# Kernel optimization log

Hardware: AMD Instinct MI355X
Metric: run time of the kernel (lower is better)

Reference implementation:

```python
import jax, jax.numpy as jnp
import numpy as np

NUM_HEADS = 8


def _forward(x, Wq, bq, Wk, bk, Wv, bv, Wo, bo, w1, b1, w2, b2, tau):
    B, S, E = x.shape
    H = NUM_HEADS
    hd = E // H
    scale = hd ** -0.5

    def heads(t):
        return t.reshape(B, S, H, hd).transpose(0, 2, 1, 3)  # [B,H,S,hd]

    q = heads(x @ Wq + bq)
    k = heads(x @ Wk + bk)
    v = heads(x @ Wv + bv)
    s = jnp.einsum('bhqd,bhkd->bhqk', q, k) * scale  # [B,H,S,S]

    # ---- autopoietic transform (vectorized over batch, no mask) ----
    s = jnp.clip(jnp.nan_to_num(s, nan=0.0, posinf=10.0, neginf=-10.0), -15.0, 15.0)
    ma = s.mean(axis=1)  # mean over heads -> [B,S,S]
    eps_safe = 0.05  # clamp(eps=1e-6, 0.05, 0.8)
    sa = jnp.clip(jnp.clip(ma, -8.0, 8.0) * eps_safe, -10.0, 10.0)
    # 1x1 conv on [1,1,S,S] == per-channel scalar scale+bias -> [B,C,S,S]
    hid = jax.nn.relu(jnp.clip(sa[:, None] * w1[None, :, None, None]
                               + b1[None, :, None, None], -5.0, 5.0))
    ap = jnp.clip(jnp.einsum('bcij,c->bij', hid, w2) + b2, -5.0, 5.0)
    taylor = jnp.clip(1.0 + 0.05 * (ap * 50.0), 0.5, 1.5)
    sig = jax.nn.sigmoid(taylor)
    p = jax.nn.softmax(jnp.clip(ma, -10.0, 10.0), axis=-1)
    Hent = -p * jnp.log(p + 1e-6)
    Fm = jax.nn.softmax(3.0 * Hent, axis=-1)
    t = sig * Fm
    eo = jnp.sqrt((ma * ma).sum(axis=(1, 2), keepdims=True)) + 1e-4  # fro norm
    et = jnp.sqrt((t * t).sum(axis=(1, 2), keepdims=True)) + 1e-4
    t = jnp.clip(eo / et, 0.8, 1.2) * t
    tm = t.mean(axis=(1, 2), keepdims=True)
    om = ma.mean(axis=(1, 2), keepdims=True)
    tstd = jnp.sqrt(jnp.clip(((t - tm) ** 2).mean(axis=(1, 2), keepdims=True), 0.01, None))
    ostd = jnp.sqrt(jnp.clip(((ma - om) ** 2).mean(axis=(1, 2), keepdims=True), 0.01, None))
    gd = jnp.clip(ostd / tstd, 0.8, 1.2)
    ar = jnp.clip(jnp.abs(ma).max(axis=(1, 2), keepdims=True), 1.0, 10.0)
    sm = jnp.clip(0.3 / jnp.log1p(ar), 0.1, 0.5)
    st = tm + sm * gd * (t - tm)  # scaled_transform
    ent = Hent.mean(axis=(1, 2), keepdims=True)
    ne = ent / jnp.log(jnp.float32(S))  # normalized entropy (max_entropy = log S)
    rr = 0.4 * (1.0 - jnp.clip(ne, 0.0, 0.4))  # residual ratio (base 0.4, entropy-damped)
    # blend transform back into per-head scores (res_scale = 1.0)
    s = s + rr[:, None] * (st - ma)[:, None]

    attn = jax.nn.softmax(s / tau, axis=-1)
    out = jnp.einsum('bhqk,bhkd->bhqd', attn, v)
    out = out.transpose(0, 2, 1, 3).reshape(B, S, E)
    return out @ Wo + bo


def setup_inputs() -> dict:
    key = jax.random.key(0)
    ks = jax.random.split(key, 8)
    B, S, E, C = 4, 512, 512, 128
    w_scale = 0.02
    return {
        'x': jax.random.normal(ks[0], (B, S, E), dtype=jnp.float32),
        'Wq': jax.random.normal(ks[1], (E, E), dtype=jnp.float32) * w_scale,
        'bq': jnp.zeros((E,), jnp.float32),
        'Wk': jax.random.normal(ks[2], (E, E), dtype=jnp.float32) * w_scale,
        'bk': jnp.zeros((E,), jnp.float32),
        'Wv': jax.random.normal(ks[3], (E, E), dtype=jnp.float32) * w_scale,
        'bv': jnp.zeros((E,), jnp.float32),
        'Wo': jax.random.normal(ks[4], (E, E), dtype=jnp.float32) * w_scale,
        'bo': jnp.zeros((E,), jnp.float32),
        'w1': jax.random.normal(ks[5], (C,), dtype=jnp.float32) * 0.5,
        'b1': jnp.zeros((C,), jnp.float32),
        'w2': jax.random.normal(ks[6], (C,), dtype=jnp.float32) * 0.1,
        'b2': jnp.zeros((1,), jnp.float32),
        'tau': jnp.ones((1,), jnp.float32),
    }


def reference(x, Wq, bq, Wk, bk, Wv, bv, Wo, bo, w1, b1, w2, b2, tau):
    return _forward(x, Wq, bq, Wk, bk, Wv, bv, Wo, bo, w1, b1, w2, b2, tau)
```

## Files before the change

kernel.cpp:

```cpp
#include <hip/hip_runtime.h>
#include <math.h>

#define BB 4
#define SS 512
#define EE 512
#define NH 8
#define HD 64
#define NC 128
#define NTAB 4096

typedef _Float16 f16x8 __attribute__((ext_vector_type(8)));
typedef float f32x4 __attribute__((ext_vector_type(4)));

struct HL { _Float16 h, l; };

__device__ __forceinline__ float clampf(float v, float lo, float hi) {
  return fminf(fmaxf(v, lo), hi);
}
__device__ __forceinline__ HL split16(float x) {
  HL r;
  r.h = (_Float16)x;
  r.l = (_Float16)(x - (float)r.h);
  return r;
}

__device__ __forceinline__ float waveRedSum(float v) {
#pragma unroll
  for (int o = 32; o; o >>= 1) v += __shfl_xor(v, o);
  return v;
}
__device__ __forceinline__ float waveRedMax(float v) {
#pragma unroll
  for (int o = 32; o; o >>= 1) v = fmaxf(v, __shfl_xor(v, o));
  return v;
}
__device__ __forceinline__ float blockRedSum(float v, float* red) {
  int tid = threadIdx.x;
  v = waveRedSum(v);
  __syncthreads();
  if ((tid & 63) == 0) red[tid >> 6] = v;
  __syncthreads();
  return red[0] + red[1] + red[2] + red[3];
}
__device__ __forceinline__ float blockRedMax(float v, float* red) {
  int tid = threadIdx.x;
  v = waveRedMax(v);
  __syncthreads();
  if ((tid & 63) == 0) red[tid >> 6] = v;
  __syncthreads();
  return fmaxf(fmaxf(red[0], red[1]), fmaxf(red[2], red[3]));
}

__global__ __launch_bounds__(256) void k_prep(
    const float* __restrict__ Wq, const float* __restrict__ Wk,
    const float* __restrict__ Wv, const float* __restrict__ Wo,
    _Float16* __restrict__ Wth, _Float16* __restrict__ Wtl) {
  const int j = blockIdx.x;
  const int tid = threadIdx.x;
  const int z = j >> 6;
  const int rem = j & 63;
  const int k0 = (rem & 7) * 64, n0 = (rem >> 3) * 64;
  const float* W = (z == 0) ? Wq : (z == 1) ? Wk : (z == 2) ? Wv : Wo;
  __shared__ float Tt[64][68];
  const int r = tid >> 2, c = (tid & 3) * 16;
#pragma unroll
  for (int jj = 0; jj < 16; jj += 4)
    *(float4*)&Tt[r][c + jj] =
        *(const float4*)(W + (size_t)(k0 + r) * EE + n0 + c + jj);
  __syncthreads();
  f16x8 h0, l0, h1, l1;
#pragma unroll
  for (int jj = 0; jj < 8; ++jj) {
    HL r0 = split16(Tt[c + jj][r]);
    HL r1 = split16(Tt[c + 8 + jj][r]);
    h0[jj] = r0.h; l0[jj] = r0.l;
    h1[jj] = r1.h; l1[jj] = r1.l;
  }
  _Float16* dh = Wth + ((size_t)z * EE + n0 + r) * EE + k0 + c;
  _Float16* dl = Wtl + ((size_t)z * EE + n0 + r) * EE + k0 + c;
  *(f16x8*)dh = h0;
  *(f16x8*)(dh + 8) = h1;
  *(f16x8*)dl = l0;
  *(f16x8*)(dl + 8) = l1;
}

__global__ __launch_bounds__(256) void k_qkv_mfma(
    const float* __restrict__ x,
    const _Float16* __restrict__ Wth, const _Float16* __restrict__ Wtl,
    const float* __restrict__ bq, const float* __restrict__ bk,
    const float* __restrict__ bv, const float* __restrict__ w1,
    const float* __restrict__ b1, const float* __restrict__ w2,
    const float* __restrict__ b2, float* __restrict__ T,
    _Float16* __restrict__ qh,
    _Float16* __restrict__ kh, _Float16* __restrict__ kl,
    _Float16* __restrict__ vth, _Float16* __restrict__ vtl) {
  const int which = blockIdx.z;
  const int tid = threadIdx.x;
  const int wave = tid >> 6, lane = tid & 63;
  const int quad = lane >> 4, l16 = lane & 15;
  const int m0 = blockIdx.y * 64;
  const int n0 = blockIdx.x * 64;
  const _Float16* Bh = Wth + (size_t)which * EE * EE;
  const _Float16* Bl = Wtl + (size_t)which * EE * EE;

  __shared__ __align__(16) char smpool[27648];
  _Float16(*LAh)[72] = (_Float16(*)[72])(smpool);
  _Float16(*LBh)[72] = (_Float16(*)[72])(smpool + 9216);
  _Float16(*LBl)[72] = (_Float16(*)[72])(smpool + 18432);
  float(*TR)[68] = (float(*)[68])(smpool);

  const int sr0 = tid >> 3, sc0 = (tid & 7) * 8;
  const int sr1 = sr0 + 32;

  float4 rx0a = *(const float4*)(x + (size_t)(m0 + sr0) * EE + sc0);
  float4 rx0b = *(const float4*)(x + (size_t)(m0 + sr0) * EE + sc0 + 4);
  float4 rx1a = *(const float4*)(x + (size_t)(m0 + sr1) * EE + sc0);
  float4 rx1b = *(const float4*)(x + (size_t)(m0 + sr1) * EE + sc0 + 4);
  f16x8 rB0h = *(const f16x8*)(Bh + (size_t)(n0 + sr0) * EE + sc0);
  f16x8 rB0l = *(const f16x8*)(Bl + (size_t)(n0 + sr0) * EE + sc0);
  f16x8 rB1h = *(const f16x8*)(Bh + (size_t)(n0 + sr1) * EE + sc0);
  f16x8 rB1l = *(const f16x8*)(Bl + (size_t)(n0 + sr1) * EE + sc0);

  f32x4 acc[4] = {};
  for (int k0 = 0; k0 < EE; k0 += 64) {
    if (k0) __syncthreads();
    {
      float f0[8] = {rx0a.x, rx0a.y, rx0a.z, rx0a.w,
                     rx0b.x, rx0b.y, rx0b.z, rx0b.w};
      float f1[8] = {rx1a.x, rx1a.y, rx1a.z, rx1a.w,
                     rx1b.x, rx1b.y, rx1b.z, rx1b.w};
      f16x8 h0, h1;
#pragma unroll
      for (int j = 0; j < 8; ++j) {
        h0[j] = (_Float16)f0[j];
        h1[j] = (_Float16)f1[j];
      }
      *(f16x8*)&LAh[sr0][sc0] = h0;
      *(f16x8*)&LAh[sr1][sc0] = h1;
    }
    *(f16x8*)&LBh[sr0][sc0] = rB0h;
    *(f16x8*)&LBl[sr0][sc0] = rB0l;
    *(f16x8*)&LBh[sr1][sc0] = rB1h;
    *(f16x8*)&LBl[sr1][sc0] = rB1l;
    __syncthreads();
    if (k0 + 64 < EE) {
      const int kn = k0 + 64;
      rx0a = *(const float4*)(x + (size_t)(m0 + sr0) * EE + kn + sc0);
      rx0b = *(const float4*)(x + (size_t)(m0 + sr0) * EE + kn + sc0 + 4);
      rx1a = *(const float4*)(x + (size_t)(m0 + sr1) * EE + kn + sc0);
      rx1b = *(const float4*)(x + (size_t)(m0 + sr1) * EE + kn + sc0 + 4);
      rB0h = *(const f16x8*)(Bh + (size_t)(n0 + sr0) * EE + kn + sc0);
      rB0l = *(const f16x8*)(Bl + (size_t)(n0 + sr0) * EE + kn + sc0);
      rB1h = *(const f16x8*)(Bh + (size_t)(n0 + sr1) * EE + kn + sc0);
      rB1l = *(const f16x8*)(Bl + (size_t)(n0 + sr1) * EE + kn + sc0);
    }
#pragma unroll
    for (int kk = 0; kk < 64; kk += 32) {
      f16x8 ah = *(const f16x8*)&LAh[wave * 16 + l16][kk + quad * 8];
#pragma unroll
      for (int nt = 0; nt < 4; ++nt) {
        f16x8 bhf = *(const f16x8*)&LBh[nt * 16 + l16][kk + quad * 8];
        f16x8 blf = *(const f16x8*)&LBl[nt * 16 + l16][kk + quad * 8];
        acc[nt] = __builtin_amdgcn_mfma_f32_16x16x32_f16(ah, bhf, acc[nt], 0, 0, 0);
        acc[nt] = __builtin_amdgcn_mfma_f32_16x16x32_f16(ah, blf, acc[nt], 0, 0, 0);
      }
    }
  }
  const float* bias = (which == 0) ? bq : (which == 1) ? bk : bv;
  if (which == 2) {
    __syncthreads();
#pragma unroll
    for (int nt = 0; nt < 4; ++nt) {
      const int dcol = nt * 16 + l16;
      const float bb = bias[n0 + nt * 16 + l16];
#pragma unroll
      for (int r = 0; r < 4; ++r)
        TR[dcol][wave * 16 + quad * 4 + r] = acc[nt][r] + bb;
    }
    __syncthreads();
    const int d = tid >> 2, cc = (tid & 3) * 16;
    const int bh = (m0 >> 9) * NH + (n0 >> 6);
    const int si0 = m0 & 511;
    f16x8 h0, l0, h1, l1;
#pragma unroll
    for (int jj = 0; jj < 8; ++jj) {
      HL r0 = split16(TR[d][cc + jj]);
      HL r1 = split16(TR[d][cc + 8 + jj]);
      h0[jj] = r0.h; l0[jj] = r0.l;
      h1[jj] = r1.h; l1[jj] = r1.l;
    }
    _Float16* dh = vth + ((size_t)bh * HD + d) * SS + si0 + cc;
    _Float16* dl = vtl + ((size_t)bh * HD + d) * SS + si0 + cc;
    *(f16x8*)dh = h0;
    *(f16x8*)(dh + 8) = h1;
    *(f16x8*)dl = l0;
    *(f16x8*)(dl + 8) = l1;
  } else {
    const float postscale = (which == 0) ? 0.125f : 1.0f;
    const int mbase = m0 + wave * 16 + quad * 4;
#pragma unroll
    for (int nt = 0; nt < 4; ++nt) {
      const int col = n0 + nt * 16 + l16;
      const float bb = bias[col];
#pragma unroll
      for (int r = 0; r < 4; ++r) {
        const size_t idx = (size_t)(mbase + r) * EE + col;
        const float val = (acc[nt][r] + bb) * postscale;
        if (which == 0) {
          qh[idx] = (_Float16)val;
        } else {
          HL sp = split16(val);
          kh[idx] = sp.h;
          kl[idx] = sp.l;
        }
      }
    }
    if (which == 0 && blockIdx.x == 0 && blockIdx.y < 17) {
      int idx = blockIdx.y * 256 + tid;
      if (idx <= NTAB) {
        float sa = -0.4f + (float)idx * (0.8f / (float)NTAB);
        float ap = 0.f;
#pragma unroll 4
        for (int c = 0; c < NC; ++c) {
          float h = fminf(fmaxf(sa * w1[c] + b1[c], 0.f), 5.f);
          ap += h * w2[c];
        }
        ap = clampf(ap + b2[0], -5.f, 5.f);
        float tay = clampf(1.0f + 0.05f * (ap * 50.0f), 0.5f, 1.5f);
        T[idx] = 1.0f / (1.0f + expf(-tay));
      }
    }
  }
}

__global__ __launch_bounds__(256) void k_ma_mfma(
    const _Float16* __restrict__ qh,
    const _Float16* __restrict__ kh, const _Float16* __restrict__ kl,
    float* __restrict__ ma) {
  const int tid = threadIdx.x;
  const int wave = tid >> 6, lane = tid & 63;
  const int quad = lane >> 4, l16 = lane & 15;
  const int m0 = blockIdx.y * 64;
  const int n0 = blockIdx.x * 64;
  const _Float16* Bh = kh + (size_t)(m0 >> 9) * SS * EE;
  const _Float16* Bl = kl + (size_t)(m0 >> 9) * SS * EE;

  __shared__ _Float16 LAh[64][72], LBh[64][72], LBl[64][72];

  const int sr0 = tid >> 3, sc0 = (tid & 7) * 8;
  const int sr1 = sr0 + 32;

  f16x8 rA0h = *(const f16x8*)(qh + (size_t)(m0 + sr0) * EE + sc0);
  f16x8 rB0h = *(const f16x8*)(Bh + (size_t)(n0 + sr0) * EE + sc0);
  f16x8 rB0l = *(const f16x8*)(Bl + (size_t)(n0 + sr0) * EE + sc0);
  f16x8 rA1h = *(const f16x8*)(qh + (size_t)(m0 + sr1) * EE + sc0);
  f16x8 rB1h = *(const f16x8*)(Bh + (size_t)(n0 + sr1) * EE + sc0);
  f16x8 rB1l = *(const f16x8*)(Bl + (size_t)(n0 + sr1) * EE + sc0);

  f32x4 acc[4] = {};
  for (int k0 = 0; k0 < EE; k0 += 64) {
    if (k0) __syncthreads();
    *(f16x8*)&LAh[sr0][sc0] = rA0h;
    *(f16x8*)&LBh[sr0][sc0] = rB0h;
    *(f16x8*)&LBl[sr0][sc0] = rB0l;
    *(f16x8*)&LAh[sr1][sc0] = rA1h;
    *(f16x8*)&LBh[sr1][sc0] = rB1h;
    *(f16x8*)&LBl[sr1][sc0] = rB1l;
    __syncthreads();
    if (k0 + 64 < EE) {
      const int kn = k0 + 64;
      rA0h = *(const f16x8*)(qh + (size_t)(m0 + sr0) * EE + kn + sc0);
      rB0h = *(const f16x8*)(Bh + (size_t)(n0 + sr0) * EE + kn + sc0);
      rB0l = *(const f16x8*)(Bl + (size_t)(n0 + sr0) * EE + kn + sc0);
      rA1h = *(const f16x8*)(qh + (size_t)(m0 + sr1) * EE + kn + sc0);
      rB1h = *(const f16x8*)(Bh + (size_t)(n0 + sr1) * EE + kn + sc0);
      rB1l = *(const f16x8*)(Bl + (size_t)(n0 + sr1) * EE + kn + sc0);
    }
#pragma unroll
    for (int kk = 0; kk < 64; kk += 32) {
      f16x8 ah = *(const f16x8*)&LAh[wave * 16 + l16][kk + quad * 8];
#pragma unroll
      for (int nt = 0; nt < 4; ++nt) {
        f16x8 bhf = *(const f16x8*)&LBh[nt * 16 + l16][kk + quad * 8];
        f16x8 blf = *(const f16x8*)&LBl[nt * 16 + l16][kk + quad * 8];
        acc[nt] = __builtin_amdgcn_mfma_f32_16x16x32_f16(ah, bhf, acc[nt], 0, 0, 0);
        acc[nt] = __builtin_amdgcn_mfma_f32_16x16x32_f16(ah, blf, acc[nt], 0, 0, 0);
      }
    }
  }
  const int mbase = m0 + wave * 16 + quad * 4;
#pragma unroll
  for (int nt = 0; nt < 4; ++nt) {
    const int col = n0 + nt * 16 + l16;
#pragma unroll
    for (int r = 0; r < 4; ++r) {
      ma[(size_t)(mbase + r) * SS + col] = acc[nt][r] * 0.125f;
    }
  }
}

__global__ __launch_bounds__(256) void k_rowstat(
    const float* __restrict__ ma, const float* __restrict__ T,
    float* __restrict__ t_un, float* __restrict__ rowred) {
  const int row = blockIdx.x * 4 + (threadIdx.x >> 6);
  const int lane = threadIdx.x & 63;

  const float4* p =
      reinterpret_cast<const float4*>(ma + (size_t)row * SS) + lane * 2;
  float4 u0 = p[0], u1 = p[1];
  float m[8] = {u0.x, u0.y, u0.z, u0.w, u1.x, u1.y, u1.z, u1.w};

  float sma = 0.f, sma2 = 0.f, mabs = 0.f;
#pragma unroll
  for (int e = 0; e < 8; ++e) {
    sma += m[e];
    sma2 += m[e] * m[e];
    mabs = fmaxf(mabs, fabsf(m[e]));
  }
  sma = waveRedSum(sma);
  sma2 = waveRedSum(sma2);
  mabs = waveRedMax(mabs);

  float ex[8], esum = 0.f;
#pragma unroll
  for (int e = 0; e < 8; ++e) {
    ex[e] = __expf(clampf(m[e], -10.f, 10.f));
    esum += ex[e];
  }
  esum = waveRedSum(esum);
  float inv = 1.0f / esum;
  float Hv[8], sH = 0.f;
#pragma unroll
  for (int e = 0; e < 8; ++e) {
    float pp = ex[e] * inv;
    Hv[e] = -pp * __logf(pp + 1e-6f);
    sH += Hv[e];
  }
  sH = waveRedSum(sH);

  float fx[8], fsum = 0.f;
#pragma unroll
  for (int e = 0; e < 8; ++e) {
    fx[e] = __expf(3.0f * Hv[e]);
    fsum += fx[e];
  }
  fsum = waveRedSum(fsum);
  float finv = 1.0f / fsum;

  float t[8], st = 0.f, st2 = 0.f;
#pragma unroll
  for (int e = 0; e < 8; ++e) {
    float sa = clampf(m[e], -8.f, 8.f) * 0.05f;
    float pos = (sa + 0.4f) * ((float)NTAB / 0.8f);
    int idx = (int)pos;
    idx = idx < 0 ? 0 : (idx > NTAB - 1 ? NTAB - 1 : idx);
    float frac = pos - (float)idx;
    float g0 = T[idx], g1 = T[idx + 1];
    float sig = g0 + (g1 - g0) * frac;
    t[e] = sig * fx[e] * finv;
    st += t[e];
    st2 += t[e] * t[e];
  }
  st = waveRedSum(st);
  st2 = waveRedSum(st2);
  {
    float4* tp = reinterpret_cast<float4*>(t_un + (size_t)row * SS) + lane * 2;
    float4 w0 = {t[0], t[1], t[2], t[3]}, w1v = {t[4], t[5], t[6], t[7]};
    tp[0] = w0;
    tp[1] = w1v;
  }
  if (lane == 0) {
    float* rp = rowred + (size_t)row * 8;
    rp[0] = sma; rp[1] = sma2; rp[2] = mabs;
    rp[3] = st;  rp[4] = st2;  rp[5] = sH;
  }
}

__global__ __launch_bounds__(256) void k_av_fused(
    const _Float16* __restrict__ qh,
    const _Float16* __restrict__ kh, const _Float16* __restrict__ kl,
    const float* __restrict__ ma, const float* __restrict__ t_un,
    const float* __restrict__ rowred, const float* __restrict__ tau,
    const _Float16* __restrict__ vth, const _Float16* __restrict__ vtl,
    _Float16* __restrict__ oh) {
  const int bh = blockIdx.y;
  const int b_ = bh >> 3, hh = bh & 7;
  const int m0 = blockIdx.x * 32;
  const int tid = threadIdx.x;
  const int wave = tid >> 6, lane = tid & 63;
  const int quad = lane >> 4, l16 = lane & 15;
  const int mt = wave >> 1, nt = wave & 1;

  __shared__ float red[4];
  float c0, c1, c2;
  {
    const float* r0 = rowred + ((size_t)b_ * SS + tid * 2) * 8;
    const float* r1 = r0 + 8;
    float sma = blockRedSum(r0[0] + r1[0], red);
    float sma2 = blockRedSum(r0[1] + r1[1], red);
    float mabs = blockRedMax(fmaxf(r0[2], r1[2]), red);
    float st = blockRedSum(r0[3] + r1[3], red);
    float st2 = blockRedSum(r0[4] + r1[4], red);
    float sH = blockRedSum(r0[5] + r1[5], red);
    const float N = (float)(SS * SS);
    float eo = sqrtf(sma2) + 1e-4f;
    float et = sqrtf(st2) + 1e-4f;
    float r = clampf(eo / et, 0.8f, 1.2f);
    float tmean = r * st / N;
    float om = sma / N;
    float vart = r * r * fmaxf(st2 / N - (st / N) * (st / N), 0.f);
    float tstd = sqrtf(fmaxf(vart, 0.01f));
    float varo = fmaxf(sma2 / N - om * om, 0.f);
    float ostd = sqrtf(fmaxf(varo, 0.01f));
    float gd = clampf(ostd / tstd, 0.8f, 1.2f);
    float ar = clampf(mabs, 1.f, 10.f);
    float sm = clampf(0.3f / log1pf(ar), 0.1f, 0.5f);
    float ent = sH / N;
    float ne = ent / logf((float)SS);
    float rr = 0.4f * (1.f - clampf(ne, 0.f, 0.4f));
    float G = sm * gd;
    c0 = rr * (1.f - G) * tmean;
    c1 = rr * G * r;
    c2 = rr;
  }
  const float itau = 1.0f / tau[0];

  __shared__ _Float16 Ph[32][40];
  __shared__ float Zp[32][2];

  const size_t qbase = (size_t)(b_ * SS + m0 + mt * 16 + l16) * EE + hh * HD;
  f16x8 a_hi[2];
#pragma unroll
  for (int ks = 0; ks < 2; ++ks)
    a_hi[ks] = *(const f16x8*)(qh + qbase + ks * 32 + quad * 8);

  const size_t kbase = (size_t)b_ * SS * EE + hh * HD;
  const size_t vbase = ((size_t)bh * HD + wave * 16 + l16) * SS;
  const size_t mb0 =
      (size_t)(b_ * SS + m0 + mt * 16 + quad * 4) * SS + nt * 16 + l16;

  f16x8 kb_h[2], kb_l[2], vb_h, vb_l;
  float mv[4], tv[4];
  {
    const size_t kr = kbase + (size_t)(nt * 16 + l16) * EE;
#pragma unroll
    for (int ks = 0; ks < 2; ++ks) {
      kb_h[ks] = *(const f16x8*)(kh + kr + ks * 32 + quad * 8);
      kb_l[ks] = *(const f16x8*)(kl + kr + ks * 32 + quad * 8);
    }
    vb_h = *(const f16x8*)(vth + vbase + quad * 8);
    vb_l = *(const f16x8*)(vtl + vbase + quad * 8);
#pragma unroll
    for (int r = 0; r < 4; ++r) {
      mv[r] = ma[mb0 + (size_t)r * SS];
      tv[r] = t_un[mb0 + (size_t)r * SS];
    }
  }

  float z[4] = {0.f, 0.f, 0.f, 0.f};
  f32x4 oacc[2] = {};
  for (int k0 = 0; k0 < SS; k0 += 32) {
    f32x4 qacc = {};
#pragma unroll
    for (int ks = 0; ks < 2; ++ks) {
      qacc = __builtin_amdgcn_mfma_f32_16x16x32_f16(a_hi[ks], kb_h[ks], qacc, 0, 0, 0);
      qacc = __builtin_amdgcn_mfma_f32_16x16x32_f16(a_hi[ks], kb_l[ks], qacc, 0, 0, 0);
    }
    const f16x8 vh_c = vb_h, vl_c = vb_l;
    __syncthreads();
#pragma unroll
    for (int r = 0; r < 4; ++r) {
      float sc = clampf(qacc[r], -15.f, 15.f);
      float v = (sc + c0 + c1 * tv[r] - c2 * mv[r]) * itau;
      float e = __expf(v) * 1.52587890625e-05f;
      z[r] += e;
      Ph[mt * 16 + quad * 4 + r][nt * 16 + l16] = (_Float16)e;
    }
    if (k0 + 32 < SS) {
      const int kn = k0 + 32;
      const size_t kr = kbase + (size_t)(kn + nt * 16 + l16) * EE;
#pragma unroll
      for (int ks = 0; ks < 2; ++ks) {
        kb_h[ks] = *(const f16x8*)(kh + kr + ks * 32 + quad * 8);
        kb_l[ks] = *(const f16x8*)(kl + kr + ks * 32 + quad * 8);
      }
      vb_h = *(const f16x8*)(vth + vbase + kn + quad * 8);
      vb_l = *(const f16x8*)(vtl + vbase + kn + quad * 8);
#pragma unroll
      for (int r = 0; r < 4; ++r) {
        mv[r] = ma[mb0 + (size_t)r * SS + kn];
        tv[r] = t_un[mb0 + (size_t)r * SS + kn];
      }
    }
    __syncthreads();
#pragma unroll
    for (int mt2 = 0; mt2 < 2; ++mt2) {
      f16x8 ah = *(const f16x8*)&Ph[mt2 * 16 + l16][quad * 8];
      oacc[mt2] = __builtin_amdgcn_mfma_f32_16x16x32_f16(ah, vh_c, oacc[mt2], 0, 0, 0);
      oacc[mt2] = __builtin_amdgcn_mfma_f32_16x16x32_f16(ah, vl_c, oacc[mt2], 0, 0, 0);
    }
  }
#pragma unroll
  for (int off = 1; off < 16; off <<= 1) {
#pragma unroll
    for (int r = 0; r < 4; ++r) z[r] += __shfl_xor(z[r], off);
  }
  if (l16 == 0) {
#pragma unroll
    for (int r = 0; r < 4; ++r) Zp[mt * 16 + quad * 4 + r][nt] = z[r];
  }
  __syncthreads();
#pragma unroll
  for (int mt2 = 0; mt2 < 2; ++mt2) {
#pragma unroll
    for (int r = 0; r < 4; ++r) {
      const int lr = mt2 * 16 + quad * 4 + r;
      const float Z = Zp[lr][0] + Zp[lr][1];
      const float oV = oacc[mt2][r] / Z;
      const int si = m0 + lr;
      const size_t idx =
          ((size_t)(b_ * SS + si)) * EE + hh * HD + wave * 16 + l16;
      oh[idx] = (_Float16)oV;
    }
  }
}

__global__ __launch_bounds__(256) void k_out_mfma(
    const _Float16* __restrict__ oh,
    const _Float16* __restrict__ Wth, const _Float16* __restrict__ Wtl,
    const float* __restrict__ bo, float* __restrict__ out) {
  const int tid = threadIdx.x;
  const int wave = tid >> 6, lane = tid & 63;
  const int quad = lane >> 4, l16 = lane & 15;
  const int m0 = blockIdx.y * 64;
  const int n0 = blockIdx.x * 64;
  const _Float16* Bh = Wth + (size_t)3 * EE * EE;
  const _Float16* Bl = Wtl + (size_t)3 * EE * EE;

  __shared__ _Float16 LAh[64][72], LBh[64][72], LBl[64][72];

  const int sr0 = tid >> 3, sc0 = (tid & 7) * 8;
  const int sr1 = sr0 + 32;

  f16x8 rA0h = *(const f16x8*)(oh + (size_t)(m0 + sr0) * EE + sc0);
  f16x8 rB0h = *(const f16x8*)(Bh + (size_t)(n0 + sr0) * EE + sc0);
  f16x8 rB0l = *(const f16x8*)(Bl + (size_t)(n0 + sr0) * EE + sc0);
  f16x8 rA1h = *(const f16x8*)(oh + (size_t)(m0 + sr1) * EE + sc0);
  f16x8 rB1h = *(const f16x8*)(Bh + (size_t)(n0 + sr1) * EE + sc0);
  f16x8 rB1l = *(const f16x8*)(Bl + (size_t)(n0 + sr1) * EE + sc0);

  f32x4 acc[4] = {};
  for (int k0 = 0; k0 < EE; k0 += 64) {
    if (k0) __syncthreads();
    *(f16x8*)&LAh[sr0][sc0] = rA0h;
    *(f16x8*)&LBh[sr0][sc0] = rB0h;
    *(f16x8*)&LBl[sr0][sc0] = rB0l;
    *(f16x8*)&LAh[sr1][sc0] = rA1h;
    *(f16x8*)&LBh[sr1][sc0] = rB1h;
    *(f16x8*)&LBl[sr1][sc0] = rB1l;
    __syncthreads();
    if (k0 + 64 < EE) {
      const int kn = k0 + 64;
      rA0h = *(const f16x8*)(oh + (size_t)(m0 + sr0) * EE + kn + sc0);
      rB0h = *(const f16x8*)(Bh + (size_t)(n0 + sr0) * EE + kn + sc0);
      rB0l = *(const f16x8*)(Bl + (size_t)(n0 + sr0) * EE + kn + sc0);
      rA1h = *(const f16x8*)(oh + (size_t)(m0 + sr1) * EE + kn + sc0);
      rB1h = *(const f16x8*)(Bh + (size_t)(n0 + sr1) * EE + kn + sc0);
      rB1l = *(const f16x8*)(Bl + (size_t)(n0 + sr1) * EE + kn + sc0);
    }
#pragma unroll
    for (int kk = 0; kk < 64; kk += 32) {
      f16x8 ah = *(const f16x8*)&LAh[wave * 16 + l16][kk + quad * 8];
#pragma unroll
      for (int nt = 0; nt < 4; ++nt) {
        f16x8 bhf = *(const f16x8*)&LBh[nt * 16 + l16][kk + quad * 8];
        f16x8 blf = *(const f16x8*)&LBl[nt * 16 + l16][kk + quad * 8];
        acc[nt] = __builtin_amdgcn_mfma_f32_16x16x32_f16(ah, bhf, acc[nt], 0, 0, 0);
        acc[nt] = __builtin_amdgcn_mfma_f32_16x16x32_f16(ah, blf, acc[nt], 0, 0, 0);
      }
    }
  }
  const int mbase = m0 + wave * 16 + quad * 4;
#pragma unroll
  for (int nt = 0; nt < 4; ++nt) {
    const int col = n0 + nt * 16 + l16;
    const float bb = bo[col];
#pragma unroll
    for (int r = 0; r < 4; ++r) {
      const int m = mbase + r;
      out[(size_t)m * EE + col] = acc[nt][r] + bb;
    }
  }
}

extern "C" void kernel_launch(void* const* d_in, const int* in_sizes, int n_in,
                              void* d_out, int out_size, void* d_ws,
                              size_t ws_size, hipStream_t stream) {
  const float* x = (const float*)d_in[0];
  const float* Wq = (const float*)d_in[1];
  const float* bq = (const float*)d_in[2];
  const float* Wk = (const float*)d_in[3];
  const float* bk = (const float*)d_in[4];
  const float* Wv = (const float*)d_in[5];
  const float* bv = (const float*)d_in[6];
  const float* Wo = (const float*)d_in[7];
  const float* bo = (const float*)d_in[8];
  const float* w1 = (const float*)d_in[9];
  const float* b1 = (const float*)d_in[10];
  const float* w2 = (const float*)d_in[11];
  const float* b2 = (const float*)d_in[12];
  const float* tau = (const float*)d_in[13];
  float* out = (float*)d_out;

  const size_t NX = (size_t)2048 * EE;
  const size_t NW = (size_t)4 * EE * EE;
  const size_t NQK = (size_t)BB * SS * EE;

  _Float16* Wth = (_Float16*)d_ws;
  _Float16* Wtl = Wth + NW;
  _Float16* qh = Wtl + NW;
  _Float16* kh = qh + NQK;
  _Float16* kl = kh + NQK;
  _Float16* vth = kl + NQK;
  _Float16* vtl = vth + NQK;
  _Float16* oh = vtl + NQK;
  float* ma = (float*)(oh + NX);
  float* t_un = ma + (size_t)BB * SS * SS;
  float* T = t_un + (size_t)BB * SS * SS;
  float* rowred = T + 8192;

  k_prep<<<256, 256, 0, stream>>>(Wq, Wk, Wv, Wo, Wth, Wtl);
  k_qkv_mfma<<<dim3(8, 32, 3), 256, 0, stream>>>(x, Wth, Wtl, bq, bk, bv, w1,
                                                 b1, w2, b2, T, qh, kh, kl,
                                                 vth, vtl);
  k_ma_mfma<<<dim3(8, 32), 256, 0, stream>>>(qh, kh, kl, ma);
  k_rowstat<<<512, 256, 0, stream>>>(ma, T, t_un, rowred);
  k_av_fused<<<dim3(16, 32), 256, 0, stream>>>(qh, kh, kl, ma, t_un,
                                               rowred, tau, vth, vtl, oh);
  k_out_mfma<<<dim3(8, 32), 256, 0, stream>>>(oh, Wth, Wtl, bo, out);
}
```

Measured before the change: 157.0 us.

## Split attention key dimension across waves with LDS reduction, halve query tile

Restructures the fused attention-value kernel so each block handles 16 query rows and each of the four waves processes a disjoint quarter of the key range (split-K). Partial outputs and softmax denominators are combined through shared memory at the end, removing the two per-iteration block barriers of the old loop. The grid doubles, giving more blocks to fill the GPU. In exchange, each block repeats the rowred block reduction, Q-tile reuse across waves is lost, and more LDS plus a final reduction pass are needed.

```diff
diff --git a/kernel.cpp b/kernel.cpp
--- a/kernel.cpp
+++ b/kernel.cpp
@@ -385,11 +385,11 @@
     _Float16* __restrict__ oh) {
   const int bh = blockIdx.y;
   const int b_ = bh >> 3, hh = bh & 7;
-  const int m0 = blockIdx.x * 32;
+  const int m0 = blockIdx.x * 16;
   const int tid = threadIdx.x;
   const int wave = tid >> 6, lane = tid & 63;
   const int quad = lane >> 4, l16 = lane & 15;
-  const int mt = wave >> 1, nt = wave & 1;
+  const int cbeg = wave * 128;
 
   __shared__ float red[4];
   float c0, c1, c2;
@@ -425,103 +425,102 @@
   }
   const float itau = 1.0f / tau[0];
 
-  __shared__ _Float16 Ph[32][40];
-  __shared__ float Zp[32][2];
-
-  const size_t qbase = (size_t)(b_ * SS + m0 + mt * 16 + l16) * EE + hh * HD;
+  __shared__ __align__(16) _Float16 Ph[4][16][40];
+  __shared__ __align__(16) float Olds[4][16][68];
+  __shared__ float Zlds[4][16];
+
+  const size_t qbase = (size_t)(b_ * SS + m0 + l16) * EE + hh * HD;
   f16x8 a_hi[2];
 #pragma unroll
   for (int ks = 0; ks < 2; ++ks)
     a_hi[ks] = *(const f16x8*)(qh + qbase + ks * 32 + quad * 8);
 
   const size_t kbase = (size_t)b_ * SS * EE + hh * HD;
-  const size_t vbase = ((size_t)bh * HD + wave * 16 + l16) * SS;
-  const size_t mb0 =
-      (size_t)(b_ * SS + m0 + mt * 16 + quad * 4) * SS + nt * 16 + l16;
-
-  f16x8 kb_h[2], kb_l[2], vb_h, vb_l;
-  float mv[4], tv[4];
+  const size_t vbase = ((size_t)bh * HD + l16) * SS;
+  const size_t mrow = (size_t)(b_ * SS + m0 + quad * 4) * SS;
+
+  float z[4] = {0.f, 0.f, 0.f, 0.f};
+  f32x4 oacc[4] = {};
+  for (int c0i = cbeg; c0i < cbeg + 128; c0i += 32) {
+    f16x8 kbh[2][2], kbl[2][2];
+#pragma unroll
+    for (int ct = 0; ct < 2; ++ct) {
+      const size_t kr = kbase + (size_t)(c0i + ct * 16 + l16) * EE;
+#pragma unroll
+      for (int ks = 0; ks < 2; ++ks) {
+        kbh[ct][ks] = *(const f16x8*)(kh + kr + ks * 32 + quad * 8);
+        kbl[ct][ks] = *(const f16x8*)(kl + kr + ks * 32 + quad * 8);
+      }
+    }
+    f16x8 vbh[4], vbl[4];
+#pragma unroll
+    for (int dt = 0; dt < 4; ++dt) {
+      const size_t vr = vbase + (size_t)(dt * 16) * SS + c0i + quad * 8;
+      vbh[dt] = *(const f16x8*)(vth + vr);
+      vbl[dt] = *(const f16x8*)(vtl + vr);
+    }
+    float mv[2][4], tv[2][4];
+#pragma unroll
+    for (int ct = 0; ct < 2; ++ct)
+#pragma unroll
+      for (int r = 0; r < 4; ++r) {
+        const size_t off = mrow + (size_t)r * SS + c0i + ct * 16 + l16;
+        mv[ct][r] = ma[off];
+        tv[ct][r] = t_un[off];
+      }
+#pragma unroll
+    for (int ct = 0; ct < 2; ++ct) {
+      f32x4 qacc = {};
+#pragma unroll
+      for (int ks = 0; ks < 2; ++ks) {
+        qacc = __builtin_amdgcn_mfma_f32_16x16x32_f16(a_hi[ks], kbh[ct][ks], qacc, 0, 0, 0);
+        qacc = __builtin_amdgcn_mfma_f32_16x16x32_f16(a_hi[ks], kbl[ct][ks], qacc, 0, 0, 0);
+      }
+#pragma unroll
+      for (int r = 0; r < 4; ++r) {
+        float sc = clampf(qacc[r], -15.f, 15.f);
+        float v = (sc + c0 + c1 * tv[ct][r] - c2 * mv[ct][r]) * itau;
+        float e = __expf(v) * 1.52587890625e-05f;
+        z[r] += e;
+        Ph[wave][quad * 4 + r][ct * 16 + l16] = (_Float16)e;
+      }
+    }
+    f16x8 pa = *(const f16x8*)&Ph[wave][l16][quad * 8];
+#pragma unroll
+    for (int dt = 0; dt < 4; ++dt) {
+      oacc[dt] = __builtin_amdgcn_mfma_f32_16x16x32_f16(pa, vbh[dt], oacc[dt], 0, 0, 0);
+      oacc[dt] = __builtin_amdgcn_mfma_f32_16x16x32_f16(pa, vbl[dt], oacc[dt], 0, 0, 0);
+    }
+  }
+#pragma unroll
+  for (int off = 1; off < 16; off <<= 1) {
+#pragma unroll
+    for (int r = 0; r < 4; ++r) z[r] += __shfl_xor(z[r], off);
+  }
+  if (l16 == 0) {
+#pragma unroll
+    for (int r = 0; r < 4; ++r) Zlds[wave][quad * 4 + r] = z[r];
+  }
+#pragma unroll
+  for (int dt = 0; dt < 4; ++dt)
+#pragma unroll
+    for (int r = 0; r < 4; ++r)
+      Olds[wave][quad * 4 + r][dt * 16 + l16] = oacc[dt][r];
+  __syncthreads();
   {
-    const size_t kr = kbase + (size_t)(nt * 16 + l16) * EE;
-#pragma unroll
-    for (int ks = 0; ks < 2; ++ks) {
-      kb_h[ks] = *(const f16x8*)(kh + kr + ks * 32 + quad * 8);
-      kb_l[ks] = *(const f16x8*)(kl + kr + ks * 32 + quad * 8);
-    }
-    vb_h = *(const f16x8*)(vth + vbase + quad * 8);
-    vb_l = *(const f16x8*)(vtl + vbase + quad * 8);
-#pragma unroll
-    for (int r = 0; r < 4; ++r) {
-      mv[r] = ma[mb0 + (size_t)r * SS];
-      tv[r] = t_un[mb0 + (size_t)r * SS];
-    }
-  }
-
-  float z[4] = {0.f, 0.f, 0.f, 0.f};
-  f32x4 oacc[2] = {};
-  for (int k0 = 0; k0 < SS; k0 += 32) {
-    f32x4 qacc = {};
-#pragma unroll
-    for (int ks = 0; ks < 2; ++ks) {
-      qacc = __builtin_amdgcn_mfma_f32_16x16x32_f16(a_hi[ks], kb_h[ks], qacc, 0, 0, 0);
-      qacc = __builtin_amdgcn_mfma_f32_16x16x32_f16(a_hi[ks], kb_l[ks], qacc, 0, 0, 0);
-    }
-    const f16x8 vh_c = vb_h, vl_c = vb_l;
-    __syncthreads();
-#pragma unroll
-    for (int r = 0; r < 4; ++r) {
-      float sc = clampf(qacc[r], -15.f, 15.f);
-      float v = (sc + c0 + c1 * tv[r] - c2 * mv[r]) * itau;
-      float e = __expf(v) * 1.52587890625e-05f;
-      z[r] += e;
-      Ph[mt * 16 + quad * 4 + r][nt * 16 + l16] = (_Float16)e;
-    }
-    if (k0 + 32 < SS) {
-      const int kn = k0 + 32;
-      const size_t kr = kbase + (size_t)(kn + nt * 16 + l16) * EE;
-#pragma unroll
-      for (int ks = 0; ks < 2; ++ks) {
-        kb_h[ks] = *(const f16x8*)(kh + kr + ks * 32 + quad * 8);
-        kb_l[ks] = *(const f16x8*)(kl + kr + ks * 32 + quad * 8);
-      }
-      vb_h = *(const f16x8*)(vth + vbase + kn + quad * 8);
-      vb_l = *(const f16x8*)(vtl + vbase + kn + quad * 8);
-#pragma unroll
-      for (int r = 0; r < 4; ++r) {
-        mv[r] = ma[mb0 + (size_t)r * SS + kn];
-        tv[r] = t_un[mb0 + (size_t)r * SS + kn];
-      }
-    }
-    __syncthreads();
-#pragma unroll
-    for (int mt2 = 0; mt2 < 2; ++mt2) {
-      f16x8 ah = *(const f16x8*)&Ph[mt2 * 16 + l16][quad * 8];
-      oacc[mt2] = __builtin_amdgcn_mfma_f32_16x16x32_f16(ah, vh_c, oacc[mt2], 0, 0, 0);
-      oacc[mt2] = __builtin_amdgcn_mfma_f32_16x16x32_f16(ah, vl_c, oacc[mt2], 0, 0, 0);
-    }
-  }
-#pragma unroll
-  for (int off = 1; off < 16; off <<= 1) {
-#pragma unroll
-    for (int r = 0; r < 4; ++r) z[r] += __shfl_xor(z[r], off);
-  }
-  if (l16 == 0) {
-#pragma unroll
-    for (int r = 0; r < 4; ++r) Zp[mt * 16 + quad * 4 + r][nt] = z[r];
-  }
-  __syncthreads();
-#pragma unroll
-  for (int mt2 = 0; mt2 < 2; ++mt2) {
-#pragma unroll
-    for (int r = 0; r < 4; ++r) {
-      const int lr = mt2 * 16 + quad * 4 + r;
-      const float Z = Zp[lr][0] + Zp[lr][1];
-      const float oV = oacc[mt2][r] / Z;
-      const int si = m0 + lr;
-      const size_t idx =
-          ((size_t)(b_ * SS + si)) * EE + hh * HD + wave * 16 + l16;
-      oh[idx] = (_Float16)oV;
-    }
+    const int row = tid >> 4;
+    const int d0 = (tid & 15) * 4;
+    float4 s0 = *(const float4*)&Olds[0][row][d0];
+    float4 s1 = *(const float4*)&Olds[1][row][d0];
+    float4 s2 = *(const float4*)&Olds[2][row][d0];
+    float4 s3 = *(const float4*)&Olds[3][row][d0];
+    float Z = Zlds[0][row] + Zlds[1][row] + Zlds[2][row] + Zlds[3][row];
+    float rz = 1.0f / Z;
+    _Float16* dst = oh + ((size_t)(b_ * SS + m0 + row)) * EE + hh * HD + d0;
+    dst[0] = (_Float16)((s0.x + s1.x + s2.x + s3.x) * rz);
+    dst[1] = (_Float16)((s0.y + s1.y + s2.y + s3.y) * rz);
+    dst[2] = (_Float16)((s0.z + s1.z + s2.z + s3.z) * rz);
+    dst[3] = (_Float16)((s0.w + s1.w + s2.w + s3.w) * rz);
   }
 }
 
@@ -635,7 +634,7 @@
                                                  vth, vtl);
   k_ma_mfma<<<dim3(8, 32), 256, 0, stream>>>(qh, kh, kl, ma);
   k_rowstat<<<512, 256, 0, stream>>>(ma, T, t_un, rowred);
-  k_av_fused<<<dim3(16, 32), 256, 0, stream>>>(qh, kh, kl, ma, t_un,
+  k_av_fused<<<dim3(32, 32), 256, 0, stream>>>(qh, kh, kl, ma, t_un,
                                                rowred, tau, vth, vtl, oh);
   k_out_mfma<<<dim3(8, 32), 256, 0, stream>>>(oh, Wth, Wtl, bo, out);
 }
```

After: 167.6 us. 1.07x slower.
